# Performance work log

Hardware: AMD Instinct MI355X
Metric: run time of the kernel (lower is better)

The kernel has to match this reference:

```python
import jax, jax.numpy as jnp
import numpy as np

B, H, L, N = 4, 256, 8192, 32  # batch, channels, seq_len, d_state//2 complex modes


def setup_inputs() -> dict:
    key = jax.random.key(0)
    ks = jax.random.split(key, 8)
    x = jax.random.normal(ks[0], (B, H, L), jnp.float32)
    # ChannelwiseLayerNorm params
    ln1_g = jnp.ones((H,), jnp.float32); ln1_b = jnp.zeros((H,), jnp.float32)
    ln2_g = jnp.ones((H,), jnp.float32); ln2_b = jnp.zeros((H,), jnp.float32)
    # S4D params (standard diagonal S4D init)
    log_dt = jax.random.uniform(ks[1], (H,), jnp.float32, np.log(1e-3), np.log(1e-1))
    log_A_real = jnp.log(0.5 * jnp.ones((H, N), jnp.float32))
    A_imag = jnp.tile(np.pi * jnp.arange(N, dtype=jnp.float32)[None, :], (H, 1))
    C_re = jax.random.normal(ks[2], (H, N), jnp.float32) * (0.5 ** 0.5)
    C_im = jax.random.normal(ks[3], (H, N), jnp.float32) * (0.5 ** 0.5)
    D = jax.random.normal(ks[4], (H,), jnp.float32)
    # 1x1 convs as dense matrices
    glu_w = jax.random.normal(ks[5], (2 * H, H), jnp.float32) * (1.0 / H) ** 0.5
    glu_b = jnp.zeros((2 * H,), jnp.float32)
    ffn_in_w = jax.random.normal(ks[6], (4 * H, H), jnp.float32) * (1.0 / H) ** 0.5
    ffn_in_b = jnp.zeros((4 * H,), jnp.float32)
    ffn_out_w = jax.random.normal(ks[7], (H, 4 * H), jnp.float32) * (1.0 / (4 * H)) ** 0.5
    ffn_out_b = jnp.zeros((H,), jnp.float32)
    return dict(x=x, ln1_g=ln1_g, ln1_b=ln1_b, ln2_g=ln2_g, ln2_b=ln2_b,
                log_dt=log_dt, log_A_real=log_A_real, A_imag=A_imag,
                C_re=C_re, C_im=C_im, D=D,
                glu_w=glu_w, glu_b=glu_b,
                ffn_in_w=ffn_in_w, ffn_in_b=ffn_in_b,
                ffn_out_w=ffn_out_w, ffn_out_b=ffn_out_b)


def _channel_ln(x, g, b, eps=1e-5):
    # normalize over channel dim (axis=1) of (B, C, L)
    mu = jnp.mean(x, axis=1, keepdims=True)
    var = jnp.var(x, axis=1, keepdims=True)
    return (x - mu) / jnp.sqrt(var + eps) * g[None, :, None] + b[None, :, None]


def _s4d(u, log_dt, log_A_real, A_imag, C_re, C_im, D):
    # u: (B, H, L); diagonal SSM via Vandermonde kernel + FFT conv
    Ls = u.shape[-1]
    dt = jnp.exp(log_dt)                       # (H,)
    A = -jnp.exp(log_A_real) + 1j * A_imag     # (H, N)
    dtA = A * dt[:, None]                      # (H, N)
    Cc = (C_re + 1j * C_im) * (jnp.exp(dtA) - 1.0) / A
    vand = jnp.exp(dtA[:, :, None] * jnp.arange(Ls))      # (H, N, L)
    K = 2.0 * jnp.einsum('hn,hnl->hl', Cc, vand).real     # (H, L)
    n = 2 * Ls
    y = jnp.fft.irfft(jnp.fft.rfft(u, n=n) * jnp.fft.rfft(K, n=n), n=n)[..., :Ls]
    return y + u * D[None, :, None]


def reference(x, ln1_g, ln1_b, ln2_g, ln2_b, log_dt, log_A_real, A_imag,
              C_re, C_im, D, glu_w, glu_b, ffn_in_w, ffn_in_b, ffn_out_w, ffn_out_b):
    # branch 1: norm -> S4D -> GELU -> 1x1 conv -> GLU -> residual
    y = _channel_ln(x, ln1_g, ln1_b)
    y = _s4d(y, log_dt, log_A_real, A_imag, C_re, C_im, D)
    y = jax.nn.gelu(y, approximate=False)
    y = jnp.einsum('oc,bcl->bol', glu_w, y) + glu_b[None, :, None]
    a, g = jnp.split(y, 2, axis=1)
    y = a * jax.nn.sigmoid(g)
    mid = x + y
    # branch 2: norm -> FFN (1x1 conv, GELU, 1x1 conv) -> residual
    y = _channel_ln(mid, ln2_g, ln2_b)
    y = jnp.einsum('oc,bcl->bol', ffn_in_w, y) + ffn_in_b[None, :, None]
    y = jax.nn.gelu(y, approximate=False)
    y = jnp.einsum('oc,bcl->bol', ffn_out_w, y) + ffn_out_b[None, :, None]
    return mid + y
```

## Files before the change

### kernel.cpp

```cpp
#include <hip/hip_runtime.h>
#include <hip/hip_bf16.h>

#define BB 4
#define HH 256
#define LL 8192
#define NN 32
#define CH 64
#define TT 128

typedef __attribute__((ext_vector_type(4))) float f32x4;
typedef __attribute__((ext_vector_type(8))) short s16x8;
typedef __attribute__((ext_vector_type(4))) short s16x4;
typedef unsigned int u32;

static __device__ __forceinline__ ushort f2bf(float f){
    union { float f; unsigned int i; } v; v.f = f;
    unsigned int x = v.i;
    return (ushort)((x + 0x7fffu + ((x >> 16) & 1u)) >> 16);
}

static __device__ __forceinline__ float fast_gelu(float x){
    float x3 = x*x*x;
    float z  = fmaf(0.03567740814f, x3, 0.7978845608f*x);
    float e  = __builtin_amdgcn_exp2f(z * 2.885390082f);
    float t  = 1.f - 2.f*__builtin_amdgcn_rcpf(e + 1.f);
    return 0.5f*x*(1.f + t);
}
static __device__ __forceinline__ float fast_sigmoid(float x){
    float e = __builtin_amdgcn_exp2f(-x * 1.442695041f);
    return __builtin_amdgcn_rcpf(1.f + e);
}

__global__ void k_prep_weights(const float* __restrict__ gw, const float* __restrict__ fiw,
                               const float* __restrict__ fow,
                               ushort* __restrict__ dglu, ushort* __restrict__ dfi,
                               ushort* __restrict__ dfo){
    int i = blockIdx.x * 256 + threadIdx.x;
    if (i < 512*256)  dglu[i] = f2bf(gw[i]);
    if (i < 1024*256) dfi[i]  = f2bf(fiw[i]);
    if (i < 1024*256) dfo[i]  = f2bf(fow[i]);
}

__global__ void k_scan_params(const float* __restrict__ log_dt, const float* __restrict__ log_A_real,
                              const float* __restrict__ A_imag, float4* __restrict__ out){
    int i = blockIdx.x * 256 + threadIdx.x;
    int h = i >> 5;
    float dt  = expf(log_dt[h]);
    float Are = -expf(log_A_real[i]);
    float Aim = A_imag[i];
    float xr = Are * dt, xi = Aim * dt;
    float er = expf(xr), sn, cs;
    sincosf(xi, &sn, &cs);
    float erT = expf(xr * (float)TT), snT, csT;
    sincosf(xi * (float)TT, &snT, &csT);
    out[i] = make_float4(er*cs, er*sn, erT*csT, erT*snT);
}

__global__ void __launch_bounds__(256) k_build(const float* __restrict__ log_dt,
      const float* __restrict__ log_A_real, const float* __restrict__ A_imag,
      const float* __restrict__ C_re, const float* __restrict__ C_im, const float* __restrict__ Dp,
      ushort* __restrict__ Tkb, ushort* __restrict__ M2b, ushort* __restrict__ V2b){
    int h = blockIdx.x, tid = threadIdx.x;
    __shared__ float prm[4][32];
    __shared__ float2 pw[129][32];
    __shared__ float kk[129];
    if (tid < 32){
        int n = tid, i = h*NN + n;
        float dt  = expf(log_dt[h]);
        float Are = -expf(log_A_real[i]);
        float Aim = A_imag[i];
        float xr = Are*dt, xi = Aim*dt;
        float er = expf(xr), sn, cs; sincosf(xi, &sn, &cs);
        float wre = er*cs, wim = er*sn;
        float nre = wre - 1.f, nim = wim;
        float inv = 1.f / (Are*Are + Aim*Aim);
        float qre = (nre*Are + nim*Aim) * inv;
        float qim = (nim*Are - nre*Aim) * inv;
        float cre = C_re[i], cim = C_im[i];
        prm[0][n] = xr; prm[1][n] = xi;
        prm[2][n] = 2.f*(cre*qre - cim*qim);
        prm[3][n] = 2.f*(cre*qim + cim*qre);
    }
    __syncthreads();
    if (tid < 129){
        float d = (float)tid, acc = 0.f;
        for (int n = 0; n < 32; ++n){
            float er = expf(prm[0][n]*d), sn, cs; sincosf(prm[1][n]*d, &sn, &cs);
            float pre = er*cs, pim = er*sn;
            pw[tid][n] = make_float2(pre, pim);
            acc += prm[2][n]*pre - prm[3][n]*pim;
        }
        kk[tid] = acc;
    }
    __syncthreads();
    float k0d = kk[0] + Dp[h];
    for (int idx = tid; idx < 128*128; idx += 256){
        int t = idx >> 7, ta = idx & 127, d = t - ta;
        float v = (d < 0) ? 0.f : ((d == 0) ? k0d : kk[d]);
        Tkb[(size_t)h*16384 + idx] = f2bf(v);
    }
    for (int idx = tid; idx < 128*64; idx += 256){
        int t = idx >> 6, j = idx & 63, n = j & 31;
        float2 p = pw[t+1][n];
        float v = (j < 32) ?  (prm[2][n]*p.x - prm[3][n]*p.y)
                           : -(prm[2][n]*p.y + prm[3][n]*p.x);
        M2b[(size_t)h*8192 + idx] = f2bf(v);
    }
    for (int idx = tid; idx < 64*128; idx += 256){
        int row = idx >> 7, ta = idx & 127, n = row & 31;
        float2 p = pw[127 - ta][n];
        V2b[(size_t)h*8192 + idx] = f2bf(row < 32 ? p.x : p.y);
    }
}

template<int MODE>
__global__ void __launch_bounds__(256) k_ln(const float* __restrict__ in, void* __restrict__ outp,
                     const float* __restrict__ gamma, const float* __restrict__ beta){
    int p = threadIdx.x & 63, cg = threadIdx.x >> 6;
    int b  = blockIdx.x / (LL/64);
    int l  = (blockIdx.x % (LL/64)) * 64 + p;
    const float* base = in + (size_t)b*HH*LL + l;
    int c0 = cg * 64;
    float s = 0.f, s2 = 0.f;
    #pragma unroll 8
    for (int j = 0; j < 64; ++j){
        float v = base[(size_t)(c0+j)*LL];
        s += v; s2 += v*v;
    }
    __shared__ float red[2][4][64];
    red[0][cg][p] = s; red[1][cg][p] = s2;
    __syncthreads();
    float ts = red[0][0][p]+red[0][1][p]+red[0][2][p]+red[0][3][p];
    float tq = red[1][0][p]+red[1][1][p]+red[1][2][p]+red[1][3][p];
    float mu   = ts * (1.f/HH);
    float var  = tq * (1.f/HH) - mu*mu;
    float rstd = rsqrtf(var + 1e-5f);
    if (MODE == 1){
        ushort* ob = (ushort*)outp + ((size_t)(b*LL + l))*HH + c0;
        #pragma unroll
        for (int j8 = 0; j8 < 8; ++j8){
            s16x8 v;
            #pragma unroll
            for (int e = 0; e < 8; ++e){
                int c = c0 + j8*8 + e;
                v[e] = (short)f2bf((base[(size_t)c*LL] - mu)*rstd*gamma[c] + beta[c]);
            }
            *(s16x8*)(ob + j8*8) = v;
        }
    } else {
        ushort* ob = (ushort*)outp + (size_t)b*HH*LL + l;
        #pragma unroll 8
        for (int j = 0; j < 64; ++j){
            int c = c0 + j;
            ob[(size_t)c*LL] = f2bf((base[(size_t)c*LL] - mu)*rstd*gamma[c] + beta[c]);
        }
    }
}

__global__ void __launch_bounds__(256) k_gemmA(const ushort* __restrict__ V2b,
                        const ushort* __restrict__ ub, float2* __restrict__ est){
    int bh = blockIdx.x, h = bh & (HH-1);
    int tid = threadIdx.x, wave = tid >> 6, lane = tid & 63;
    int m16 = lane & 15, kg = lane >> 4;
    const ushort* Vh = V2b + (size_t)h*8192;
    const ushort* ux = ub + (size_t)bh*LL;
    f32x4 acc[4] = {};
    #pragma unroll
    for (int k0 = 0; k0 < 128; k0 += 32){
        s16x8 fa = *(const s16x8*)&Vh[(wave*16 + m16)*128 + k0 + kg*8];
        #pragma unroll
        for (int nf = 0; nf < 4; ++nf){
            s16x8 fb = *(const s16x8*)&ux[(size_t)(nf*16 + m16)*128 + k0 + kg*8];
            acc[nf] = __builtin_amdgcn_mfma_f32_16x16x32_bf16(fa, fb, acc[nf], 0, 0, 0);
        }
    }
    #pragma unroll
    for (int nf = 0; nf < 4; ++nf){
        int c = nf*16 + m16;
        #pragma unroll
        for (int r = 0; r < 4; ++r){
            int srow = wave*16 + kg*4 + r;
            float* dst = (float*)&est[((size_t)bh*CH + c)*NN + (srow & 31)];
            dst[srow >> 5] = acc[nf][r];
        }
    }
}

__global__ void k_scan_B(const float4* __restrict__ par, const float2* __restrict__ est,
                         ushort* __restrict__ carr){
    int i = blockIdx.x * 256 + threadIdx.x;
    int n = i & 31, bh = i >> 5, h = bh & (HH-1);
    float4 p0 = par[h*NN + n];
    float wre = p0.z, wim = p0.w;
    float cre = 0.f, cim = 0.f;
    const float2* e = est + (size_t)bh*CH*NN + n;
    ushort* cb = carr + (size_t)bh*CH*64;
    for (int c = 0; c < CH; ++c){
        cb[c*64 + n]      = f2bf(cre);
        cb[c*64 + 32 + n] = f2bf(cim);
        float2 v = e[(size_t)c*NN];
        float nre = fmaf(wre, cre, fmaf(-wim, cim, v.x));
        float nim = fmaf(wre, cim, fmaf(wim, cre, v.y));
        cre = nre; cim = nim;
    }
}

__global__ void __launch_bounds__(256) k_gemmC(const ushort* __restrict__ Tkb,
                        const ushort* __restrict__ M2b, const ushort* __restrict__ ub,
                        const ushort* __restrict__ carr, ushort* __restrict__ gy){
    int bh = blockIdx.x, h = bh & (HH-1);
    int tid = threadIdx.x, wave = tid >> 6, lane = tid & 63;
    int m16 = lane & 15, kg = lane >> 4;
    const ushort* Th = Tkb + (size_t)h*16384;
    const ushort* Mh = M2b + (size_t)h*8192;
    const ushort* ux = ub + (size_t)bh*LL;
    const ushort* cb = carr + (size_t)bh*CH*64;
    f32x4 acc[2][4] = {};
    #pragma unroll
    for (int k0 = 0; k0 < 128; k0 += 32){
        s16x8 fa0 = *(const s16x8*)&Th[(size_t)(wave*32 + m16)*128 + k0 + kg*8];
        s16x8 fa1 = *(const s16x8*)&Th[(size_t)(wave*32 + 16 + m16)*128 + k0 + kg*8];
        #pragma unroll
        for (int nf = 0; nf < 4; ++nf){
            s16x8 fb = *(const s16x8*)&ux[(size_t)(nf*16 + m16)*128 + k0 + kg*8];
            acc[0][nf] = __builtin_amdgcn_mfma_f32_16x16x32_bf16(fa0, fb, acc[0][nf], 0, 0, 0);
            acc[1][nf] = __builtin_amdgcn_mfma_f32_16x16x32_bf16(fa1, fb, acc[1][nf], 0, 0, 0);
        }
    }
    #pragma unroll
    for (int k0 = 0; k0 < 64; k0 += 32){
        s16x8 fa0 = *(const s16x8*)&Mh[(wave*32 + m16)*64 + k0 + kg*8];
        s16x8 fa1 = *(const s16x8*)&Mh[(wave*32 + 16 + m16)*64 + k0 + kg*8];
        #pragma unroll
        for (int nf = 0; nf < 4; ++nf){
            s16x8 fb = *(const s16x8*)&cb[(nf*16 + m16)*64 + k0 + kg*8];
            acc[0][nf] = __builtin_amdgcn_mfma_f32_16x16x32_bf16(fa0, fb, acc[0][nf], 0, 0, 0);
            acc[1][nf] = __builtin_amdgcn_mfma_f32_16x16x32_bf16(fa1, fb, acc[1][nf], 0, 0, 0);
        }
    }
    #pragma unroll
    for (int mf = 0; mf < 2; ++mf){
        #pragma unroll
        for (int nf = 0; nf < 4; ++nf){
            int c = nf*16 + m16;
            int t0 = wave*32 + mf*16 + kg*4;
            s16x4 pk;
            #pragma unroll
            for (int r = 0; r < 4; ++r){
                pk[r] = (short)f2bf(fast_gelu(acc[mf][nf][r]));
            }
            *(s16x4*)&gy[(size_t)bh*LL + c*TT + t0] = pk;
        }
    }
}

__global__ void k_transpose(const ushort* __restrict__ in, ushort* __restrict__ out){
    __shared__ ushort tile[64][66];
    int tid = threadIdx.x;
    int lt = blockIdx.x, ht = blockIdx.y, b = blockIdx.z;
    const ushort* ib = in + ((size_t)b*HH + ht*64)*LL + lt*64;
    #pragma unroll
    for (int k = 0; k < 16; ++k){
        int j = tid + k*256;
        tile[j >> 6][j & 63] = ib[(size_t)(j >> 6)*LL + (j & 63)];
    }
    __syncthreads();
    ushort* obp = out + ((size_t)b*LL + lt*64)*HH + ht*64;
    #pragma unroll
    for (int k = 0; k < 16; ++k){
        int j = tid + k*256;
        obp[(size_t)(j >> 6)*HH + (j & 63)] = tile[j & 63][j >> 6];
    }
}

__global__ void __launch_bounds__(256) k_glu(const ushort* __restrict__ Wg, const ushort* __restrict__ Xt,
                     const float* __restrict__ x, const float* __restrict__ gb,
                     float* __restrict__ mid){
    __shared__ __align__(16) ushort sh[32768];
    int tid = threadIdx.x;
    int w = tid >> 6, lane = tid & 63;
    int m16 = lane & 15, kg = lane >> 4;
    int wr = w >> 1, wc = w & 1;
    int p0  = blockIdx.x * 128;
    int oa0 = blockIdx.y * 64;
    const ushort* Brow = Xt + (size_t)p0*256;
    int srow = lane >> 3, scol = (lane & 7)*8;
    f32x4 aa[2][4] = {}; f32x4 ag[2][4] = {};

    #define GSTAGE(buf, kt) { \
        int k0s = (kt)*64; \
        _Pragma("unroll") \
        for (int i = 0; i < 4; ++i){ \
            int rr = (w*4 + i)*8; \
            int grow = (rr < 64) ? (oa0 + rr + srow) : (256 + oa0 + (rr - 64) + srow); \
            __builtin_amdgcn_global_load_lds( \
                (const __attribute__((address_space(1))) u32*)(Wg + (size_t)grow*256 + k0s + scol), \
                (__attribute__((address_space(3))) u32*)&sh[(buf)*8192 + rr*64], 16, 0, 0); \
            __builtin_amdgcn_global_load_lds( \
                (const __attribute__((address_space(1))) u32*)(Brow + (size_t)(rr + srow)*256 + k0s + scol), \
                (__attribute__((address_space(3))) u32*)&sh[16384 + (buf)*8192 + rr*64], 16, 0, 0); \
        } }

    int buf = 0;
    GSTAGE(0, 0);
    __syncthreads();
    for (int kt = 0; kt < 4; ++kt){
        if (kt + 1 < 4) GSTAGE(buf^1, kt+1);
        #pragma unroll
        for (int k032 = 0; k032 < 64; k032 += 32){
            s16x8 fa[2], fg[2], fb[4];
            #pragma unroll
            for (int i = 0; i < 2; ++i){
                fa[i] = *(const s16x8*)&sh[buf*8192 + (wr*32 + i*16 + m16)*64 + k032 + kg*8];
                fg[i] = *(const s16x8*)&sh[buf*8192 + (64 + wr*32 + i*16 + m16)*64 + k032 + kg*8];
            }
            #pragma unroll
            for (int i = 0; i < 4; ++i)
                fb[i] = *(const s16x8*)&sh[16384 + buf*8192 + (wc*64 + i*16 + m16)*64 + k032 + kg*8];
            #pragma unroll
            for (int mf = 0; mf < 2; ++mf){
                #pragma unroll
                for (int nf = 0; nf < 4; ++nf){
                    aa[mf][nf] = __builtin_amdgcn_mfma_f32_16x16x32_bf16(fa[mf], fb[nf], aa[mf][nf], 0, 0, 0);
                    ag[mf][nf] = __builtin_amdgcn_mfma_f32_16x16x32_bf16(fg[mf], fb[nf], ag[mf][nf], 0, 0, 0);
                }
            }
        }
        __syncthreads();
        buf ^= 1;
    }
    #undef GSTAGE

    #pragma unroll
    for (int mf = 0; mf < 2; ++mf){
        #pragma unroll
        for (int nf = 0; nf < 4; ++nf){
            int pc = p0 + wc*64 + nf*16 + m16;
            int b = pc >> 13, l = pc & (LL-1);
            #pragma unroll
            for (int r = 0; r < 4; ++r){
                int o = oa0 + wr*32 + mf*16 + kg*4 + r;
                float va  = aa[mf][nf][r] + gb[o];
                float vg  = ag[mf][nf][r] + gb[o + 256];
                float sig = fast_sigmoid(vg);
                size_t idx = ((size_t)(b*HH + o) << 13) + l;
                mid[idx] = x[idx] + va*sig;
            }
        }
    }
}

template<int KDIM, int EPI>
__global__ void __launch_bounds__(256) k_gemm_lds(const ushort* __restrict__ A,
                      const ushort* __restrict__ Bm, const float* __restrict__ bias,
                      const float* __restrict__ mid, void* __restrict__ Cout, int pbase){
    __shared__ __align__(16) ushort sh[35072];
    int tid = threadIdx.x;
    int w = tid >> 6, lane = tid & 63;
    int m16 = lane & 15, kg = lane >> 4;
    int wr = w >> 1, wc = w & 1;
    int q0  = blockIdx.x * 128;
    int oc0 = blockIdx.y * 128;
    const ushort* Arow = A  + (size_t)oc0*KDIM;
    const ushort* Brow = Bm + (size_t)q0*KDIM;
    int srow = lane >> 3, scol = (lane & 7)*8;
    f32x4 acc[4][4] = {};
    const int nK = KDIM/64;

    #define STAGE(buf, kt) { \
        int k0s = (kt)*64; \
        _Pragma("unroll") \
        for (int i = 0; i < 4; ++i){ \
            int rr = (w*4 + i)*8; \
            __builtin_amdgcn_global_load_lds( \
                (const __attribute__((address_space(1))) u32*)(Arow + (size_t)(rr + srow)*KDIM + k0s + scol), \
                (__attribute__((address_space(3))) u32*)&sh[(buf)*8192 + rr*64], 16, 0, 0); \
            __builtin_amdgcn_global_load_lds( \
                (const __attribute__((address_space(1))) u32*)(Brow + (size_t)(rr + srow)*KDIM + k0s + scol), \
                (__attribute__((address_space(3))) u32*)&sh[16384 + (buf)*8192 + rr*64], 16, 0, 0); \
        } }

    int buf = 0;
    STAGE(0, 0);
    __syncthreads();
    for (int kt = 0; kt < nK; ++kt){
        if (kt + 1 < nK) STAGE(buf^1, kt+1);
        #pragma unroll
        for (int k032 = 0; k032 < 64; k032 += 32){
            s16x8 af[4], bf[4];
            #pragma unroll
            for (int i = 0; i < 4; ++i){
                af[i] = *(const s16x8*)&sh[buf*8192 + (wr*64 + i*16 + m16)*64 + k032 + kg*8];
                bf[i] = *(const s16x8*)&sh[16384 + buf*8192 + (wc*64 + i*16 + m16)*64 + k032 + kg*8];
            }
            #pragma unroll
            for (int mf = 0; mf < 4; ++mf){
                #pragma unroll
                for (int nf = 0; nf < 4; ++nf)
                    acc[mf][nf] = __builtin_amdgcn_mfma_f32_16x16x32_bf16(af[mf], bf[nf], acc[mf][nf], 0, 0, 0);
            }
        }
        __syncthreads();
        buf ^= 1;
    }
    #undef STAGE

    if (EPI == 0){
        ushort (*lt)[136] = (ushort(*)[136])sh;
        #pragma unroll
        for (int mf = 0; mf < 4; ++mf){
            #pragma unroll
            for (int nf = 0; nf < 4; ++nf){
                int lr = wc*64 + nf*16 + m16;
                int lc = wr*64 + mf*16 + kg*4;
                s16x4 pk;
                #pragma unroll
                for (int r = 0; r < 4; ++r){
                    float v = acc[mf][nf][r] + bias[oc0 + lc + r];
                    pk[r] = (short)f2bf(fast_gelu(v));
                }
                *(s16x4*)&lt[lr][lc] = pk;
            }
        }
        __syncthreads();
        ushort* f1 = (ushort*)Cout;
        #pragma unroll
        for (int i = 0; i < 8; ++i){
            int chunk = i*256 + tid;
            int row = chunk >> 4, c16 = chunk & 15;
            s16x8 v = *(const s16x8*)&lt[row][c16*8];
            *(s16x8*)&f1[((size_t)(q0 + row) << 10) + oc0 + c16*8] = v;
        }
    } else {
        float* out = (float*)Cout;
        #pragma unroll
        for (int mf = 0; mf < 4; ++mf){
            #pragma unroll
            for (int nf = 0; nf < 4; ++nf){
                int pc = pbase + q0 + wc*64 + nf*16 + m16;
                int b = pc >> 13, l = pc & (LL-1);
                #pragma unroll
                for (int r = 0; r < 4; ++r){
                    int oc = oc0 + wr*64 + mf*16 + kg*4 + r;
                    size_t idx = ((size_t)(b*HH + oc) << 13) + l;
                    out[idx] = mid[idx] + acc[mf][nf][r] + bias[oc];
                }
            }
        }
    }
}

extern "C" void kernel_launch(void* const* d_in, const int* in_sizes, int n_in,
                              void* d_out, int out_size, void* d_ws, size_t ws_size,
                              hipStream_t stream) {
    const float* x          = (const float*)d_in[0];
    const float* ln1_g      = (const float*)d_in[1];
    const float* ln1_b      = (const float*)d_in[2];
    const float* ln2_g      = (const float*)d_in[3];
    const float* ln2_b      = (const float*)d_in[4];
    const float* log_dt     = (const float*)d_in[5];
    const float* log_A_real = (const float*)d_in[6];
    const float* A_imag     = (const float*)d_in[7];
    const float* C_re       = (const float*)d_in[8];
    const float* C_im       = (const float*)d_in[9];
    const float* Dv         = (const float*)d_in[10];
    const float* glu_w      = (const float*)d_in[11];
    const float* glu_b      = (const float*)d_in[12];
    const float* ffn_in_w   = (const float*)d_in[13];
    const float* ffn_in_b   = (const float*)d_in[14];
    const float* ffn_out_w  = (const float*)d_in[15];
    const float* ffn_out_b  = (const float*)d_in[16];
    float* out = (float*)d_out;

    char* ws = (char*)d_ws;
    const size_t MB = 1u << 20;
    float4* par  = (float4*)(ws);
    ushort* wglu = (ushort*)(ws + 256*1024);
    ushort* wfi  = (ushort*)(ws + 512*1024);
    ushort* wfo  = (ushort*)(ws + 1024*1024);
    ushort* Tkb  = (ushort*)(ws + 2*MB);
    ushort* M2b  = (ushort*)(ws + 10*MB);
    ushort* V2b  = (ushort*)(ws + 14*MB);
    ushort* ub   = (ushort*)(ws + 18*MB);
    float2* est  = (float2*)(ws + 34*MB);
    ushort* carr = (ushort*)(ws + 50*MB);
    ushort* gy   = (ushort*)(ws + 34*MB);
    ushort* gyt  = (ushort*)(ws + 50*MB);
    float*  mid  = (float*)(ws + 2*MB);
    ushort* x2t  = (ushort*)(ws + 36*MB);
    ushort* f1   = (ushort*)(ws + 52*MB);

    int G = (ws_size >= 117*MB) ? 4 : ((ws_size >= 85*MB) ? 2 : 1);

    k_prep_weights<<<1024, 256, 0, stream>>>(glu_w, ffn_in_w, ffn_out_w, wglu, wfi, wfo);
    k_scan_params<<<32, 256, 0, stream>>>(log_dt, log_A_real, A_imag, par);
    k_build<<<HH, 256, 0, stream>>>(log_dt, log_A_real, A_imag, C_re, C_im, Dv, Tkb, M2b, V2b);
    k_ln<2><<<BB*LL/64, 256, 0, stream>>>(x, ub, ln1_g, ln1_b);
    k_gemmA<<<BB*HH, 256, 0, stream>>>(V2b, ub, est);
    k_scan_B<<<BB*HH*NN/256, 256, 0, stream>>>(par, est, carr);
    k_gemmC<<<BB*HH, 256, 0, stream>>>(Tkb, M2b, ub, carr, gy);
    k_transpose<<<dim3(LL/64, HH/64, BB), 256, 0, stream>>>(gy, gyt);
    k_glu<<<dim3(BB*LL/128, 4), 256, 0, stream>>>(wglu, gyt, x, glu_b, mid);
    k_ln<1><<<BB*LL/64, 256, 0, stream>>>(mid, x2t, ln2_g, ln2_b);
    for (int b0 = 0; b0 < BB; b0 += G){
        int pbase = b0 * LL;
        k_gemm_lds<256,0><<<dim3(G*LL/128, 8), 256, 0, stream>>>(
            wfi, x2t + (size_t)pbase*256, ffn_in_b, nullptr, f1, 0);
        k_gemm_lds<1024,1><<<dim3(G*LL/128, 2), 256, 0, stream>>>(
            wfo, f1, ffn_out_b, mid, out, pbase);
    }
    (void)in_sizes; (void)n_in; (void)out_size; (void)ws_size;
}
```

Measured before the change: 305.3 us.

## XOR-swizzle LDS tiles and drop double buffering in GLU and FFN GEMMs

Applies an XOR swizzle to the 16-byte column chunks both when staging A/B tiles into LDS and when reading MFMA fragments, to avoid LDS bank conflicts on the row-strided fragment reads. It also removes the double-buffered prefetch, replacing it with single-buffered load, sync, compute, sync, which halves LDS usage so more blocks may fit per CU. The trade-off is that global-to-LDS loads no longer overlap with MFMA compute within a block, so latency hiding now depends on occupancy.

After: 323.3 us. 5.9% more time.

```diff
diff --git a/kernel.cpp b/kernel.cpp
--- a/kernel.cpp
+++ b/kernel.cpp
@@ -276,7 +276,7 @@
 __global__ void __launch_bounds__(256) k_glu(const ushort* __restrict__ Wg, const ushort* __restrict__ Xt,
                      const float* __restrict__ x, const float* __restrict__ gb,
                      float* __restrict__ mid){
-    __shared__ __align__(16) ushort sh[32768];
+    __shared__ __align__(16) ushort sh[16384];
     int tid = threadIdx.x;
     int w = tid >> 6, lane = tid & 63;
     int m16 = lane & 15, kg = lane >> 4;
@@ -284,39 +284,40 @@
     int p0  = blockIdx.x * 128;
     int oa0 = blockIdx.y * 64;
     const ushort* Brow = Xt + (size_t)p0*256;
-    int srow = lane >> 3, scol = (lane & 7)*8;
+    int srow = lane >> 3;
+    int scol = ((lane & 7) ^ (srow & 7)) * 8;
     f32x4 aa[2][4] = {}; f32x4 ag[2][4] = {};
 
-    #define GSTAGE(buf, kt) { \
-        int k0s = (kt)*64; \
-        _Pragma("unroll") \
-        for (int i = 0; i < 4; ++i){ \
-            int rr = (w*4 + i)*8; \
-            int grow = (rr < 64) ? (oa0 + rr + srow) : (256 + oa0 + (rr - 64) + srow); \
-            __builtin_amdgcn_global_load_lds( \
-                (const __attribute__((address_space(1))) u32*)(Wg + (size_t)grow*256 + k0s + scol), \
-                (__attribute__((address_space(3))) u32*)&sh[(buf)*8192 + rr*64], 16, 0, 0); \
-            __builtin_amdgcn_global_load_lds( \
-                (const __attribute__((address_space(1))) u32*)(Brow + (size_t)(rr + srow)*256 + k0s + scol), \
-                (__attribute__((address_space(3))) u32*)&sh[16384 + (buf)*8192 + rr*64], 16, 0, 0); \
-        } }
-
-    int buf = 0;
-    GSTAGE(0, 0);
-    __syncthreads();
     for (int kt = 0; kt < 4; ++kt){
-        if (kt + 1 < 4) GSTAGE(buf^1, kt+1);
+        int k0s = kt*64;
+        #pragma unroll
+        for (int i = 0; i < 4; ++i){
+            int rr = (w*4 + i)*8;
+            int grow = (rr < 64) ? (oa0 + rr + srow) : (256 + oa0 + (rr - 64) + srow);
+            __builtin_amdgcn_global_load_lds(
+                (const __attribute__((address_space(1))) u32*)(Wg + (size_t)grow*256 + k0s + scol),
+                (__attribute__((address_space(3))) u32*)&sh[rr*64], 16, 0, 0);
+            __builtin_amdgcn_global_load_lds(
+                (const __attribute__((address_space(1))) u32*)(Brow + (size_t)(rr + srow)*256 + k0s + scol),
+                (__attribute__((address_space(3))) u32*)&sh[8192 + rr*64], 16, 0, 0);
+        }
+        __syncthreads();
         #pragma unroll
         for (int k032 = 0; k032 < 64; k032 += 32){
+            int c = (k032 >> 3) + kg;
             s16x8 fa[2], fg[2], fb[4];
             #pragma unroll
             for (int i = 0; i < 2; ++i){
-                fa[i] = *(const s16x8*)&sh[buf*8192 + (wr*32 + i*16 + m16)*64 + k032 + kg*8];
-                fg[i] = *(const s16x8*)&sh[buf*8192 + (64 + wr*32 + i*16 + m16)*64 + k032 + kg*8];
-            }
-            #pragma unroll
-            for (int i = 0; i < 4; ++i)
-                fb[i] = *(const s16x8*)&sh[16384 + buf*8192 + (wc*64 + i*16 + m16)*64 + k032 + kg*8];
+                int ra = wr*32 + i*16 + m16;
+                int rg = 64 + wr*32 + i*16 + m16;
+                fa[i] = *(const s16x8*)&sh[ra*64 + ((c ^ (ra & 7)) << 3)];
+                fg[i] = *(const s16x8*)&sh[rg*64 + ((c ^ (rg & 7)) << 3)];
+            }
+            #pragma unroll
+            for (int i = 0; i < 4; ++i){
+                int rb = wc*64 + i*16 + m16;
+                fb[i] = *(const s16x8*)&sh[8192 + rb*64 + ((c ^ (rb & 7)) << 3)];
+            }
             #pragma unroll
             for (int mf = 0; mf < 2; ++mf){
                 #pragma unroll
@@ -327,9 +328,7 @@
             }
         }
         __syncthreads();
-        buf ^= 1;
-    }
-    #undef GSTAGE
+    }
 
     #pragma unroll
     for (int mf = 0; mf < 2; ++mf){
@@ -354,7 +353,7 @@
 __global__ void __launch_bounds__(256) k_gemm_lds(const ushort* __restrict__ A,
                       const ushort* __restrict__ Bm, const float* __restrict__ bias,
                       const float* __restrict__ mid, void* __restrict__ Cout, int pbase){
-    __shared__ __align__(16) ushort sh[35072];
+    __shared__ __align__(16) ushort sh[17408];
     int tid = threadIdx.x;
     int w = tid >> 6, lane = tid & 63;
     int m16 = lane & 15, kg = lane >> 4;
@@ -363,35 +362,34 @@
     int oc0 = blockIdx.y * 128;
     const ushort* Arow = A  + (size_t)oc0*KDIM;
     const ushort* Brow = Bm + (size_t)q0*KDIM;
-    int srow = lane >> 3, scol = (lane & 7)*8;
+    int srow = lane >> 3;
+    int scol = ((lane & 7) ^ (srow & 7)) * 8;
     f32x4 acc[4][4] = {};
     const int nK = KDIM/64;
 
-    #define STAGE(buf, kt) { \
-        int k0s = (kt)*64; \
-        _Pragma("unroll") \
-        for (int i = 0; i < 4; ++i){ \
-            int rr = (w*4 + i)*8; \
-            __builtin_amdgcn_global_load_lds( \
-                (const __attribute__((address_space(1))) u32*)(Arow + (size_t)(rr + srow)*KDIM + k0s + scol), \
-                (__attribute__((address_space(3))) u32*)&sh[(buf)*8192 + rr*64], 16, 0, 0); \
-            __builtin_amdgcn_global_load_lds( \
-                (const __attribute__((address_space(1))) u32*)(Brow + (size_t)(rr + srow)*KDIM + k0s + scol), \
-                (__attribute__((address_space(3))) u32*)&sh[16384 + (buf)*8192 + rr*64], 16, 0, 0); \
-        } }
-
-    int buf = 0;
-    STAGE(0, 0);
-    __syncthreads();
     for (int kt = 0; kt < nK; ++kt){
-        if (kt + 1 < nK) STAGE(buf^1, kt+1);
+        int k0s = kt*64;
+        #pragma unroll
+        for (int i = 0; i < 4; ++i){
+            int rr = (w*4 + i)*8;
+            __builtin_amdgcn_global_load_lds(
+                (const __attribute__((address_space(1))) u32*)(Arow + (size_t)(rr + srow)*KDIM + k0s + scol),
+                (__attribute__((address_space(3))) u32*)&sh[rr*64], 16, 0, 0);
+            __builtin_amdgcn_global_load_lds(
+                (const __attribute__((address_space(1))) u32*)(Brow + (size_t)(rr + srow)*KDIM + k0s + scol),
+                (__attribute__((address_space(3))) u32*)&sh[8192 + rr*64], 16, 0, 0);
+        }
+        __syncthreads();
         #pragma unroll
         for (int k032 = 0; k032 < 64; k032 += 32){
+            int c = (k032 >> 3) + kg;
             s16x8 af[4], bf[4];
             #pragma unroll
             for (int i = 0; i < 4; ++i){
-                af[i] = *(const s16x8*)&sh[buf*8192 + (wr*64 + i*16 + m16)*64 + k032 + kg*8];
-                bf[i] = *(const s16x8*)&sh[16384 + buf*8192 + (wc*64 + i*16 + m16)*64 + k032 + kg*8];
+                int ra = wr*64 + i*16 + m16;
+                int rb = wc*64 + i*16 + m16;
+                af[i] = *(const s16x8*)&sh[ra*64 + ((c ^ (ra & 7)) << 3)];
+                bf[i] = *(const s16x8*)&sh[8192 + rb*64 + ((c ^ (rb & 7)) << 3)];
             }
             #pragma unroll
             for (int mf = 0; mf < 4; ++mf){
@@ -401,9 +399,7 @@
             }
         }
         __syncthreads();
-        buf ^= 1;
-    }
-    #undef STAGE
+    }
 
     if (EPI == 0){
         ushort (*lt)[136] = (ushort(*)[136])sh;
```
